# Kernel optimization log

Measured on AMD Instinct MI355X. Metric: run time of the kernel, lower is better.

## Reference

```python
import jax, jax.numpy as jnp
import numpy as np

B, S, F, H = 4, 1024, 256, 8
SCALE = float(F) ** 0.5  # source MULTIPLIES logits by sqrt(f)


def setup_inputs() -> dict:
    key = jax.random.key(0)
    ks = jax.random.split(key, 5)
    # 0.02 init scale keeps sigmoid logits in a non-saturated range
    return {
        "q_input": jax.random.normal(ks[0], (B, S, F), dtype=jnp.float32),
        "Wq": jax.random.normal(ks[1], (F, F * H), dtype=jnp.float32) * 0.02,
        "Wk": jax.random.normal(ks[2], (F, F * H), dtype=jnp.float32) * 0.02,
        "Wv": jax.random.normal(ks[3], (F, F * H), dtype=jnp.float32) * 0.02,
        "Wo": jax.random.normal(ks[4], (F * H, F), dtype=jnp.float32) * 0.02,
    }


def reference(q_input, Wq, Wk, Wv, Wo):
    b, s, f = q_input.shape
    h = Wq.shape[1] // f
    # kv_input is None in source -> self-attention (kv = q_input)
    q = (q_input.reshape(b * s, f) @ Wq).reshape(b, s, f, h)
    k = (q_input.reshape(b * s, f) @ Wk).reshape(b, s, f, h)
    v = (q_input.reshape(b * s, f) @ Wv).reshape(b, s, f, h)
    qkt = jnp.einsum('bifh,bjfh->bijh', q, k)          # [b, i, j, h]
    attn = jax.nn.sigmoid(qkt * SCALE)                  # sigmoid, NOT softmax
    wv = jnp.einsum('bijh,bjfh->bifh', attn, v)         # [b, i, f, h]
    wv = wv.reshape(b * s, f * h)
    out = jax.nn.relu(wv @ Wo)                          # projection + ReLU
    return out.reshape(b, s, f)
```

## Files before the change

kernel.cpp:

```cpp
#include <hip/hip_runtime.h>
#include <math.h>

#define SQ 1024
#define FQ 256
#define FH 2048

typedef _Float16 f16;
typedef f16  f16x8 __attribute__((ext_vector_type(8)));
typedef float f32x4 __attribute__((ext_vector_type(4)));

#define GLOAD_LDS16(gp, lp) \
    __builtin_amdgcn_global_load_lds((const __attribute__((address_space(1))) void*)(gp), \
                                     (__attribute__((address_space(3))) void*)(lp), 16, 0, 0)

#define SIG16(s) __builtin_amdgcn_rcpf(1.0f + __builtin_amdgcn_exp2f(-23.083120654223414f * (s)))

__global__ __launch_bounds__(256) void prep_kernel(const float* __restrict__ x,
                                                   const float* __restrict__ Wq,
                                                   const float* __restrict__ Wk,
                                                   const float* __restrict__ Wv,
                                                   const float* __restrict__ Wo,
                                                   f16* __restrict__ xh,
                                                   f16* __restrict__ wqT,
                                                   f16* __restrict__ wkT,
                                                   f16* __restrict__ wvT,
                                                   f16* __restrict__ woT) {
    const int z = blockIdx.z;
    if (z == 4) {
        int id = (int)(blockIdx.x * 8 + blockIdx.y);
        int idx = (id * 256 + (int)threadIdx.x) * 8;
        float4 a = *(const float4*)(x + idx);
        float4 b = *(const float4*)(x + idx + 4);
        f16x8 v = {(f16)a.x, (f16)a.y, (f16)a.z, (f16)a.w,
                   (f16)b.x, (f16)b.y, (f16)b.z, (f16)b.w};
        *(f16x8*)(xh + idx) = v;
        return;
    }
    __shared__ f16 T[32][33];
    const int tx = threadIdx.x & 31, ty = threadIdx.x >> 5;
    if (z < 3) {
        const float* W = z == 0 ? Wq : (z == 1 ? Wk : Wv);
        f16* WT        = z == 0 ? wqT : (z == 1 ? wkT : wvT);
        const int n0 = blockIdx.x * 32, k0 = blockIdx.y * 32;
#pragma unroll
        for (int i = 0; i < 4; ++i)
            T[ty + i * 8][tx] = (f16)W[(size_t)(k0 + ty + i * 8) * FH + n0 + tx];
        __syncthreads();
#pragma unroll
        for (int i = 0; i < 4; ++i)
            WT[(size_t)(n0 + ty + i * 8) * FQ + k0 + tx] = T[tx][ty + i * 8];
    } else {
        const int n0 = (blockIdx.x >> 3) * 32;
        const int yy = (blockIdx.x & 7) * 8 + blockIdx.y;
        const int ft = yy >> 3, h = yy & 7;
#pragma unroll
        for (int i = 0; i < 4; ++i) {
            int fl = ty + i * 8;
            T[fl][tx] = (f16)Wo[(size_t)((ft * 32 + fl) * 8 + h) * FQ + n0 + tx];
        }
        __syncthreads();
#pragma unroll
        for (int i = 0; i < 4; ++i)
            woT[(size_t)(n0 + ty + i * 8) * FH + h * 256 + ft * 32 + tx] = T[tx][ty + i * 8];
    }
}

__device__ __forceinline__ void stage_sw64(const f16* __restrict__ G, int ldg,
                                           int row0, int c0, f16* S,
                                           int nrows, int w, int lane) {
    const int rsub = lane >> 3;
    const int g    = (lane & 7) ^ (rsub & 7);
#pragma unroll
    for (int rI = w; rI < (nrows >> 3); rI += 4) {
        GLOAD_LDS16(G + (size_t)(row0 + rI * 8 + rsub) * ldg + c0 + g * 8,
                    S + rI * 512);
    }
}

__device__ __forceinline__ void gemm128_sw(const f16* __restrict__ A, int lda,
                                           const f16* __restrict__ Bt, int ldb,
                                           int kbeg, int kend, f16* As, f16* Bs,
                                           f32x4 acc[4][4], int row0, int col0) {
    const int t = threadIdx.x, lane = t & 63, w = t >> 6;
    const int wr = w >> 1, wc = w & 1;
    const int lrow = lane & 15, quad = lane >> 4;
    for (int k0 = kbeg; k0 < kend; k0 += 64) {
        __syncthreads();
        stage_sw64(A, lda, row0, k0, As, 128, w, lane);
        stage_sw64(Bt, ldb, col0, k0, Bs, 128, w, lane);
        __syncthreads();
#pragma unroll
        for (int kk = 0; kk < 2; ++kk) {
            f16x8 af[4], bf[4];
#pragma unroll
            for (int i = 0; i < 4; ++i) {
                int r = wr * 64 + i * 16 + lrow;
                af[i] = *(const f16x8*)&As[r * 64 + (((kk * 4 + quad) ^ (r & 7)) << 3)];
            }
#pragma unroll
            for (int j = 0; j < 4; ++j) {
                int r = wc * 64 + j * 16 + lrow;
                bf[j] = *(const f16x8*)&Bs[r * 64 + (((kk * 4 + quad) ^ (r & 7)) << 3)];
            }
#pragma unroll
            for (int i = 0; i < 4; ++i)
#pragma unroll
                for (int j = 0; j < 4; ++j)
                    acc[i][j] = __builtin_amdgcn_mfma_f32_16x16x32_f16(af[i], bf[j], acc[i][j], 0, 0, 0);
        }
    }
}

__global__ __launch_bounds__(256) void proj_mfma(const f16* __restrict__ xh,
                                                 const f16* __restrict__ wqT,
                                                 const f16* __restrict__ wkT,
                                                 const f16* __restrict__ wvT,
                                                 f16* __restrict__ qb,
                                                 f16* __restrict__ kb,
                                                 f16* __restrict__ vb) {
    const int z = blockIdx.z;
    const f16* WT = z == 0 ? wqT : (z == 1 ? wkT : wvT);
    f16* O        = z == 0 ? qb  : (z == 1 ? kb  : vb);
    __shared__ f16 smem[17408];
    f16* As = smem;
    f16* Bs = smem + 8192;
    f32x4 acc[4][4] = {};
    const int row0 = blockIdx.y * 128, col0 = blockIdx.x * 128;
    gemm128_sw(xh, FQ, WT, FQ, 0, FQ, As, Bs, acc, row0, col0);

    __syncthreads();
    f16* Es = smem;
    const int lane = threadIdx.x & 63, w = threadIdx.x >> 6;
    const int wr = w >> 1, wc = w & 1;
    const int lrow = lane & 15, quad = lane >> 4;
    if (z != 2) {
#pragma unroll
        for (int i = 0; i < 4; ++i)
#pragma unroll
            for (int rr = 0; rr < 4; ++rr) {
                int rl = 64 * wr + 16 * i + 4 * quad + rr;
#pragma unroll
                for (int j = 0; j < 4; ++j) {
                    int cc = 64 * wc + 16 * j + lrow;
                    Es[rl * 136 + (cc & 7) * 16 + (cc >> 3)] = (f16)acc[i][j][rr];
                }
            }
        __syncthreads();
        const int f0 = col0 >> 3;
#pragma unroll
        for (int it = 0; it < 4; ++it) {
            int c = it * 256 + threadIdx.x;
            int row = c >> 3, hh = c & 7;
            int gr = row0 + row, bbb = gr >> 10, s = gr & 1023;
            f16x8 v0 = *(const f16x8*)&Es[row * 136 + hh * 16];
            f16x8 v1 = *(const f16x8*)&Es[row * 136 + hh * 16 + 8];
            f16* dst = O + ((size_t)(bbb * 8 + hh) * SQ + s) * FQ + f0;
            *(f16x8*)dst = v0;
            *(f16x8*)(dst + 8) = v1;
        }
    } else {
#pragma unroll
        for (int i = 0; i < 4; ++i)
#pragma unroll
            for (int rr = 0; rr < 4; ++rr) {
                int rl = 64 * wr + 16 * i + 4 * quad + rr;
#pragma unroll
                for (int j = 0; j < 4; ++j) {
                    int cc = 64 * wc + 16 * j + lrow;
                    Es[cc * 136 + rl] = (f16)acc[i][j][rr];
                }
            }
        __syncthreads();
        const int bbb = row0 >> 10, s0 = row0 & 1023;
#pragma unroll
        for (int it = 0; it < 8; ++it) {
            int c = it * 256 + threadIdx.x;
            int cc = c >> 4, sc = c & 15;
            int hh = cc & 7, f = (col0 >> 3) + (cc >> 3);
            f16x8 v = *(const f16x8*)&Es[cc * 136 + sc * 8];
            *(f16x8*)(O + ((size_t)(bbb * 8 + hh) * FQ + f) * SQ + s0 + sc * 8) = v;
        }
    }
}

__global__ __launch_bounds__(256) void fused_attn(const f16* __restrict__ Qb,
                                                  const f16* __restrict__ Kb,
                                                  const f16* __restrict__ Vt,
                                                  f16* __restrict__ WV) {
    __shared__ f16 smem[35328];
    const int t = threadIdx.x, lane = t & 63, w = t >> 6;
    const int lrow = lane & 15, quad = lane >> 4;
    f16* Pw = smem + 32768 + w * 640;
    const int n = blockIdx.x;
    const int xcd = n & 7, rest = n >> 3;
    const int bh = xcd * 4 + (rest & 3);
    const int strip = rest >> 2;
    const int m0 = strip * 64;
    const int bb = bh >> 3, h = bh & 7;
    const f16* Qg = Qb + (size_t)bh * SQ * FQ;
    const f16* Kg = Kb + (size_t)bh * SQ * FQ;
    const f16* Vg = Vt + (size_t)bh * FQ * SQ;

    f16x8 qf[8];
#pragma unroll
    for (int ks = 0; ks < 8; ++ks)
        qf[ks] = *(const f16x8*)(Qg + (size_t)(m0 + 16 * w + lrow) * FQ + ks * 32 + quad * 8);

    const int krs = lane >> 5;
    const int kgp = lane & 31;
    const int vrs = lane >> 2;
    const int vgp = lane & 3;

#pragma unroll
    for (int i = 0; i < 4; ++i) {
        int rI = w + i * 4;
        int r = rI * 2 + krs;
        GLOAD_LDS16(Kg + (size_t)r * FQ + ((kgp ^ (r & 7)) << 3), smem + rI * 512);
    }
#pragma unroll
    for (int i = 0; i < 4; ++i) {
        int rI = w + i * 4;
        int f = rI * 16 + vrs;
        GLOAD_LDS16(Vg + (size_t)f * SQ + ((vgp ^ ((f >> 1) & 3)) << 3),
                    smem + 16384 + rI * 512);
    }

    f32x4 acc_o[16] = {};

    for (int jt = 0; jt < 32; ++jt) {
        const int j0 = jt * 32;
        f16* KBc = (jt & 1) ? smem + 8192  : smem;
        f16* VBc = (jt & 1) ? smem + 24576 : smem + 16384;
        __syncthreads();
        if (jt < 31) {
            f16* KBn = (jt & 1) ? smem         : smem + 8192;
            f16* VBn = (jt & 1) ? smem + 16384 : smem + 24576;
#pragma unroll
            for (int i = 0; i < 4; ++i) {
                int rI = w + i * 4;
                int r = rI * 2 + krs;
                GLOAD_LDS16(Kg + (size_t)(j0 + 32 + r) * FQ + ((kgp ^ (r & 7)) << 3),
                            KBn + rI * 512);
            }
#pragma unroll
            for (int i = 0; i < 4; ++i) {
                int rI = w + i * 4;
                int f = rI * 16 + vrs;
                GLOAD_LDS16(Vg + (size_t)f * SQ + j0 + 32 + ((vgp ^ ((f >> 1) & 3)) << 3),
                            VBn + rI * 512);
            }
        }
        f32x4 acc_s[2] = {};
#pragma unroll
        for (int ks = 0; ks < 8; ++ks) {
#pragma unroll
            for (int nj = 0; nj < 2; ++nj) {
                int rk = 16 * nj + lrow;
                f16x8 bf = *(const f16x8*)&KBc[rk * 256 + (((ks * 4 + quad) ^ (rk & 7)) << 3)];
                acc_s[nj] = __builtin_amdgcn_mfma_f32_16x16x32_f16(qf[ks], bf, acc_s[nj], 0, 0, 0);
            }
        }
#pragma unroll
        for (int nj = 0; nj < 2; ++nj)
#pragma unroll
            for (int rr = 0; rr < 4; ++rr)
                Pw[(4 * quad + rr) * 40 + 16 * nj + lrow] = (f16)SIG16(acc_s[nj][rr]);
        f16x8 ap = *(const f16x8*)&Pw[lrow * 40 + quad * 8];
#pragma unroll
        for (int nj = 0; nj < 16; ++nj) {
            int f = 16 * nj + lrow;
            f16x8 bv = *(const f16x8*)&VBc[f * 32 + ((quad ^ ((f >> 1) & 3)) << 3)];
            acc_o[nj] = __builtin_amdgcn_mfma_f32_16x16x32_f16(ap, bv, acc_o[nj], 0, 0, 0);
        }
    }
    __syncthreads();
    f16* Es = smem;
#pragma unroll
    for (int nj = 0; nj < 16; ++nj)
#pragma unroll
        for (int rr = 0; rr < 4; ++rr)
            Es[(16 * w + 4 * quad + rr) * 264 + 16 * nj + lrow] = (f16)acc_o[nj][rr];
    __syncthreads();
#pragma unroll
    for (int it = 0; it < 8; ++it) {
        int c = it * 256 + t;
        int r = c >> 5, ck = c & 31;
        f16x8 v = *(const f16x8*)&Es[r * 264 + ck * 8];
        *(f16x8*)(WV + (size_t)(bb * SQ + m0 + r) * FH + h * 256 + ck * 8) = v;
    }
}

__global__ __launch_bounds__(256) void out_mfma8(const f16* __restrict__ WVm,
                                                 const f16* __restrict__ WoT,
                                                 float* __restrict__ PP) {
    __shared__ f16 smem[16384];
    f16* As = smem;
    f16* Bs = smem + 8192;
    f32x4 acc[4][4] = {};
    const int row0 = blockIdx.y * 128, col0 = blockIdx.x * 128;
    const int kbeg = blockIdx.z * 256;
    gemm128_sw(WVm, FH, WoT, FH, kbeg, kbeg + 256, As, Bs, acc, row0, col0);

    float* P = PP + (size_t)blockIdx.z * SQ * 4 * FQ;
    const int lane = threadIdx.x & 63, w = threadIdx.x >> 6;
    const int wr = w >> 1, wc = w & 1;
    const int lrow = lane & 15, quad = lane >> 4;
#pragma unroll
    for (int i = 0; i < 4; ++i)
#pragma unroll
        for (int rr = 0; rr < 4; ++rr) {
            int gr = row0 + wr * 64 + i * 16 + quad * 4 + rr;
#pragma unroll
            for (int j = 0; j < 4; ++j) {
                int gc = col0 + wc * 64 + j * 16 + lrow;
                P[(size_t)gr * FQ + gc] = acc[i][j][rr];
            }
        }
}

__global__ __launch_bounds__(256) void reduce_relu8(const float* __restrict__ PP,
                                                    float* __restrict__ O) {
    int idx = (blockIdx.x * 256 + threadIdx.x) * 4;
    f32x4 s = *(const f32x4*)(PP + idx);
#pragma unroll
    for (int z = 1; z < 8; ++z)
        s += *(const f32x4*)(PP + (size_t)z * 1048576 + idx);
    f32x4 r = {fmaxf(s.x, 0.f), fmaxf(s.y, 0.f), fmaxf(s.z, 0.f), fmaxf(s.w, 0.f)};
    *(f32x4*)(O + idx) = r;
}

extern "C" void kernel_launch(void* const* d_in, const int* in_sizes, int n_in,
                              void* d_out, int out_size, void* d_ws, size_t ws_size,
                              hipStream_t stream) {
    const float* x  = (const float*)d_in[0];
    const float* Wq = (const float*)d_in[1];
    const float* Wk = (const float*)d_in[2];
    const float* Wv = (const float*)d_in[3];
    const float* Wo = (const float*)d_in[4];
    float* out = (float*)d_out;

    f16* ws = (f16*)d_ws;
    f16* xh    = ws;
    f16* wqT   = xh    + 1048576;
    f16* wkT   = wqT   + 524288;
    f16* wvT   = wkT   + 524288;
    f16* woT   = wvT   + 524288;
    f16* qbuf  = woT   + 524288;
    f16* kbuf  = qbuf  + 8388608;
    f16* vbuf  = kbuf  + 8388608;
    f16* wvbuf = vbuf  + 8388608;
    float* pp  = (float*)qbuf;

    dim3 blk(256);
    prep_kernel<<<dim3(64, 8, 5), blk, 0, stream>>>(x, Wq, Wk, Wv, Wo,
                                                    xh, wqT, wkT, wvT, woT);

    proj_mfma<<<dim3(16, 32, 3), blk, 0, stream>>>(xh, wqT, wkT, wvT, qbuf, kbuf, vbuf);

    fused_attn<<<dim3(512), blk, 0, stream>>>(qbuf, kbuf, vbuf, wvbuf);

    out_mfma8<<<dim3(2, 32, 8), blk, 0, stream>>>(wvbuf, woT, pp);
    reduce_relu8<<<dim3(1024), blk, 0, stream>>>(pp, out);
}
```

Measured before the change: 184.4 us.

## Double query rows per wave in fused attention to reuse K/V fragments

Each wave in fused_attn now computes two 16-row query tiles (32 rows), so every block covers 128 query rows and the grid shrinks from 512 to 256 blocks. Each K and V fragment read from LDS now feeds two MFMAs, and each block's K/V global-to-LDS traffic serves twice as many rows. This is meant to cut LDS reads and global K/V traffic per unit of work. The cost is more accumulator registers (launch_bounds set to one block per CU) and fewer resident waves to hide latency, since there is now only one 4-wave block per CU.

```diff
diff --git a/kernel.cpp b/kernel.cpp
--- a/kernel.cpp
+++ b/kernel.cpp
@@ -183,28 +183,31 @@
     }
 }
 
-__global__ __launch_bounds__(256) void fused_attn(const f16* __restrict__ Qb,
-                                                  const f16* __restrict__ Kb,
-                                                  const f16* __restrict__ Vt,
-                                                  f16* __restrict__ WV) {
-    __shared__ f16 smem[35328];
+__global__ __launch_bounds__(256, 1) void fused_attn(const f16* __restrict__ Qb,
+                                                     const f16* __restrict__ Kb,
+                                                     const f16* __restrict__ Vt,
+                                                     f16* __restrict__ WV) {
+    __shared__ f16 smem[37888];
     const int t = threadIdx.x, lane = t & 63, w = t >> 6;
     const int lrow = lane & 15, quad = lane >> 4;
-    f16* Pw = smem + 32768 + w * 640;
+    f16* Pw = smem + 32768 + w * 1280;
     const int n = blockIdx.x;
     const int xcd = n & 7, rest = n >> 3;
     const int bh = xcd * 4 + (rest & 3);
     const int strip = rest >> 2;
-    const int m0 = strip * 64;
+    const int m0 = strip * 128;
     const int bb = bh >> 3, h = bh & 7;
     const f16* Qg = Qb + (size_t)bh * SQ * FQ;
     const f16* Kg = Kb + (size_t)bh * SQ * FQ;
     const f16* Vg = Vt + (size_t)bh * FQ * SQ;
 
-    f16x8 qf[8];
-#pragma unroll
-    for (int ks = 0; ks < 8; ++ks)
-        qf[ks] = *(const f16x8*)(Qg + (size_t)(m0 + 16 * w + lrow) * FQ + ks * 32 + quad * 8);
+    f16x8 qf[2][8];
+#pragma unroll
+    for (int mi = 0; mi < 2; ++mi)
+#pragma unroll
+        for (int ks = 0; ks < 8; ++ks)
+            qf[mi][ks] = *(const f16x8*)(Qg + (size_t)(m0 + 32 * w + 16 * mi + lrow) * FQ
+                                             + ks * 32 + quad * 8);
 
     const int krs = lane >> 5;
     const int kgp = lane & 31;
@@ -225,7 +228,7 @@
                     smem + 16384 + rI * 512);
     }
 
-    f32x4 acc_o[16] = {};
+    f32x4 acc_o[2][16] = {};
 
     for (int jt = 0; jt < 32; ++jt) {
         const int j0 = jt * 32;
@@ -250,39 +253,57 @@
                             VBn + rI * 512);
             }
         }
-        f32x4 acc_s[2] = {};
+        f32x4 acc_s[2][2] = {};
 #pragma unroll
         for (int ks = 0; ks < 8; ++ks) {
+            f16x8 bf[2];
 #pragma unroll
             for (int nj = 0; nj < 2; ++nj) {
                 int rk = 16 * nj + lrow;
-                f16x8 bf = *(const f16x8*)&KBc[rk * 256 + (((ks * 4 + quad) ^ (rk & 7)) << 3)];
-                acc_s[nj] = __builtin_amdgcn_mfma_f32_16x16x32_f16(qf[ks], bf, acc_s[nj], 0, 0, 0);
-            }
-        }
-#pragma unroll
-        for (int nj = 0; nj < 2; ++nj)
-#pragma unroll
-            for (int rr = 0; rr < 4; ++rr)
-                Pw[(4 * quad + rr) * 40 + 16 * nj + lrow] = (f16)SIG16(acc_s[nj][rr]);
-        f16x8 ap = *(const f16x8*)&Pw[lrow * 40 + quad * 8];
+                bf[nj] = *(const f16x8*)&KBc[rk * 256 + (((ks * 4 + quad) ^ (rk & 7)) << 3)];
+            }
+#pragma unroll
+            for (int mi = 0; mi < 2; ++mi)
+#pragma unroll
+                for (int nj = 0; nj < 2; ++nj)
+                    acc_s[mi][nj] = __builtin_amdgcn_mfma_f32_16x16x32_f16(
+                        qf[mi][ks], bf[nj], acc_s[mi][nj], 0, 0, 0);
+        }
+#pragma unroll
+        for (int mi = 0; mi < 2; ++mi)
+#pragma unroll
+            for (int nj = 0; nj < 2; ++nj)
+#pragma unroll
+                for (int rr = 0; rr < 4; ++rr)
+                    Pw[(16 * mi + 4 * quad + rr) * 40 + 16 * nj + lrow] =
+                        (f16)SIG16(acc_s[mi][nj][rr]);
+        f16x8 ap[2];
+#pragma unroll
+        for (int mi = 0; mi < 2; ++mi)
+            ap[mi] = *(const f16x8*)&Pw[(16 * mi + lrow) * 40 + quad * 8];
 #pragma unroll
         for (int nj = 0; nj < 16; ++nj) {
             int f = 16 * nj + lrow;
             f16x8 bv = *(const f16x8*)&VBc[f * 32 + ((quad ^ ((f >> 1) & 3)) << 3)];
-            acc_o[nj] = __builtin_amdgcn_mfma_f32_16x16x32_f16(ap, bv, acc_o[nj], 0, 0, 0);
+#pragma unroll
+            for (int mi = 0; mi < 2; ++mi)
+                acc_o[mi][nj] = __builtin_amdgcn_mfma_f32_16x16x32_f16(
+                    ap[mi], bv, acc_o[mi][nj], 0, 0, 0);
         }
     }
     __syncthreads();
     f16* Es = smem;
 #pragma unroll
-    for (int nj = 0; nj < 16; ++nj)
-#pragma unroll
-        for (int rr = 0; rr < 4; ++rr)
-            Es[(16 * w + 4 * quad + rr) * 264 + 16 * nj + lrow] = (f16)acc_o[nj][rr];
+    for (int mi = 0; mi < 2; ++mi)
+#pragma unroll
+        for (int nj = 0; nj < 16; ++nj)
+#pragma unroll
+            for (int rr = 0; rr < 4; ++rr)
+                Es[(32 * w + 16 * mi + 4 * quad + rr) * 264 + 16 * nj + lrow] =
+                    (f16)acc_o[mi][nj][rr];
     __syncthreads();
 #pragma unroll
-    for (int it = 0; it < 8; ++it) {
+    for (int it = 0; it < 16; ++it) {
         int c = it * 256 + t;
         int r = c >> 5, ck = c & 31;
         f16x8 v = *(const f16x8*)&Es[r * 264 + ck * 8];
@@ -357,7 +378,7 @@
 
     proj_mfma<<<dim3(16, 32, 3), blk, 0, stream>>>(xh, wqT, wkT, wvT, qbuf, kbuf, vbuf);
 
-    fused_attn<<<dim3(512), blk, 0, stream>>>(qbuf, kbuf, vbuf, wvbuf);
+    fused_attn<<<dim3(256), blk, 0, stream>>>(qbuf, kbuf, vbuf, wvbuf);
 
     out_mfma8<<<dim3(2, 32, 8), blk, 0, stream>>>(wvbuf, woT, pp);
     reduce_relu8<<<dim3(1024), blk, 0, stream>>>(pp, out);
```

New measurement: 182.6 us. About the same (-0.9%).
